# Kernel optimization log

Hardware: AMD Instinct MI355X
Metric: run time of the kernel (lower is better)

The kernel has to match this reference:

```python
import jax, jax.numpy as jnp
import numpy as np

EPS = 1e-8  # numerical guard in padded (masked) softmax denominator


def setup_inputs() -> dict:
    key = jax.random.key(0)
    k1, k2 = jax.random.split(key)
    B, N, D = 8, 2048, 3
    coordinates = jax.random.normal(k1, (B, N, D), dtype=jnp.float32)
    masks = (jax.random.uniform(k2, (B, N, N)) < 0.9).astype(jnp.float32)
    sigma = jnp.ones((1,), dtype=jnp.float32)  # NonNeg learned scalar
    return {"coordinates": coordinates, "masks": masks, "sigma": sigma}


def reference(coordinates, masks, sigma):
    # pairwise squared euclidean distances: ||xi||^2 - 2 xi.xj + ||xj||^2
    norms = jnp.sum(coordinates ** 2, axis=-1, keepdims=True)            # [B,N,1]
    inner = jnp.einsum('bnd,bmd->bnm', coordinates, coordinates)         # [B,N,N]
    distances = norms - 2.0 * inner + jnp.swapaxes(norms, -1, -2)        # [B,N,N]
    # Gaussian kernel
    A = jnp.exp(-distances / (sigma ** 2))                               # [B,N,N]
    # padded_softmax: mask then row-normalize (A is positive, so this is a
    # masked softmax over -d/sigma^2 along the last axis)
    A = A * masks
    return A / (jnp.sum(A, axis=-1, keepdims=True) + EPS)
```

## Files before the change

kernel.cpp:

```cpp
#include <hip/hip_runtime.h>
#include <math.h>


#define NN 2048
#define THREADS 256
#define RPB 8
#define EPS 1e-8f

typedef float nfloat4 __attribute__((ext_vector_type(4)));

__global__ __launch_bounds__(THREADS) void gauss_adj_kernel(
    const float* __restrict__ coords,
    const float* __restrict__ masks,
    const float* __restrict__ sigma,
    float* __restrict__ out)
{
    const int rows_base = blockIdx.x * RPB;
    const int b   = rows_base >> 11;
    const int ib  = rows_base & (NN - 1);
    const int tid = threadIdx.x;
    const int wave = tid >> 6;
    const int lane = tid & 63;

    __shared__ float srow[RPB * 3];
    __shared__ float red[2][4];

    const float* cb = coords + (size_t)b * NN * 3;
    if (tid < RPB * 3) srow[tid] = cb[ib * 3 + tid];

    const float4* cb4 = (const float4*)cb;
    float xs[2][4], ys[2][4], zs[2][4];
    #pragma unroll
    for (int c = 0; c < 2; ++c) {
        const int j4 = c * THREADS + tid;
        const float4 f0 = cb4[3 * j4 + 0];
        const float4 f1 = cb4[3 * j4 + 1];
        const float4 f2 = cb4[3 * j4 + 2];
        xs[c][0] = f0.x; ys[c][0] = f0.y; zs[c][0] = f0.z;
        xs[c][1] = f0.w; ys[c][1] = f1.x; zs[c][1] = f1.y;
        xs[c][2] = f1.z; ys[c][2] = f1.w; zs[c][2] = f2.x;
        xs[c][3] = f2.y; ys[c][3] = f2.z; zs[c][3] = f2.w;
    }

    const float s = sigma[0];
    const float inv_s2 = 1.0f / (s * s);

    __syncthreads();

    for (int r = 0; r < RPB; ++r) {
        const int row = rows_base + r;
        const float xi = srow[r * 3 + 0];
        const float yi = srow[r * 3 + 1];
        const float zi = srow[r * 3 + 2];

        const float4* mrow = (const float4*)(masks + (size_t)row * NN);

        float vals[2][4];
        float lsum = 0.0f;
        #pragma unroll
        for (int c = 0; c < 2; ++c) {
            const float4 m = mrow[c * THREADS + tid];
            const float mm[4] = {m.x, m.y, m.z, m.w};
            #pragma unroll
            for (int q = 0; q < 4; ++q) {
                const float dx = xi - xs[c][q];
                const float dy = yi - ys[c][q];
                const float dz = zi - zs[c][q];
                const float a = __expf(-(dx * dx + dy * dy + dz * dz) * inv_s2) * mm[q];
                vals[c][q] = a;
                lsum += a;
            }
        }

        #pragma unroll
        for (int off = 1; off < 64; off <<= 1)
            lsum += __shfl_xor(lsum, off, 64);
        if (lane == 0) red[r & 1][wave] = lsum;
        __syncthreads();
        const float tot = red[r & 1][0] + red[r & 1][1] + red[r & 1][2] + red[r & 1][3];
        const float inv = 1.0f / (tot + EPS);

        nfloat4* orow = (nfloat4*)(out + (size_t)row * NN);
        #pragma unroll
        for (int c = 0; c < 2; ++c) {
            nfloat4 o;
            o.x = vals[c][0] * inv;
            o.y = vals[c][1] * inv;
            o.z = vals[c][2] * inv;
            o.w = vals[c][3] * inv;
            __builtin_nontemporal_store(o, &orow[c * THREADS + tid]);
        }
    }
}

extern "C" void kernel_launch(void* const* d_in, const int* in_sizes, int n_in,
                              void* d_out, int out_size, void* d_ws, size_t ws_size,
                              hipStream_t stream) {
    const float* coords = (const float*)d_in[0];
    const float* masks  = (const float*)d_in[1];
    const float* sigma  = (const float*)d_in[2];
    float* out = (float*)d_out;

    const int B = in_sizes[0] / (NN * 3);
    const int rows = B * NN;
    gauss_adj_kernel<<<rows / RPB, THREADS, 0, stream>>>(coords, masks, sigma, out);
}
```

Before: 243.5 us.

## Batch row reductions into one barrier and recompute exps in a second pass

```diff
diff --git a/kernel.cpp b/kernel.cpp
--- a/kernel.cpp
+++ b/kernel.cpp
@@ -23,7 +23,7 @@
     const int lane = tid & 63;
 
     __shared__ float srow[RPB * 3];
-    __shared__ float red[2][4];
+    __shared__ float red[4][RPB];
 
     const float* cb = coords + (size_t)b * NN * 3;
     if (tid < RPB * 3) srow[tid] = cb[ib * 3 + tid];
@@ -47,47 +47,69 @@
 
     __syncthreads();
 
+    const float4* mbase = (const float4*)(masks + (size_t)rows_base * NN);
+
+    float lsum[RPB];
+    #pragma unroll
+    for (int r = 0; r < RPB; ++r) lsum[r] = 0.0f;
+
+    #pragma unroll
     for (int r = 0; r < RPB; ++r) {
-        const int row = rows_base + r;
         const float xi = srow[r * 3 + 0];
         const float yi = srow[r * 3 + 1];
         const float zi = srow[r * 3 + 2];
-
-        const float4* mrow = (const float4*)(masks + (size_t)row * NN);
-
-        float vals[2][4];
-        float lsum = 0.0f;
         #pragma unroll
         for (int c = 0; c < 2; ++c) {
-            const float4 m = mrow[c * THREADS + tid];
+            const float4 m = mbase[r * (NN / 4) + c * THREADS + tid];
             const float mm[4] = {m.x, m.y, m.z, m.w};
             #pragma unroll
             for (int q = 0; q < 4; ++q) {
                 const float dx = xi - xs[c][q];
                 const float dy = yi - ys[c][q];
                 const float dz = zi - zs[c][q];
-                const float a = __expf(-(dx * dx + dy * dy + dz * dz) * inv_s2) * mm[q];
-                vals[c][q] = a;
-                lsum += a;
+                lsum[r] += __expf(-(dx * dx + dy * dy + dz * dz) * inv_s2) * mm[q];
             }
         }
+    }
 
+    #pragma unroll
+    for (int r = 0; r < RPB; ++r) {
         #pragma unroll
         for (int off = 1; off < 64; off <<= 1)
-            lsum += __shfl_xor(lsum, off, 64);
-        if (lane == 0) red[r & 1][wave] = lsum;
-        __syncthreads();
-        const float tot = red[r & 1][0] + red[r & 1][1] + red[r & 1][2] + red[r & 1][3];
-        const float inv = 1.0f / (tot + EPS);
+            lsum[r] += __shfl_xor(lsum[r], off, 64);
+    }
+    if (lane == 0) {
+        #pragma unroll
+        for (int r = 0; r < RPB; ++r) red[wave][r] = lsum[r];
+    }
+    __syncthreads();
 
-        nfloat4* orow = (nfloat4*)(out + (size_t)row * NN);
+    float invv[RPB];
+    #pragma unroll
+    for (int r = 0; r < RPB; ++r)
+        invv[r] = 1.0f / (red[0][r] + red[1][r] + red[2][r] + red[3][r] + EPS);
+
+    #pragma unroll
+    for (int r = 0; r < RPB; ++r) {
+        const float xi = srow[r * 3 + 0];
+        const float yi = srow[r * 3 + 1];
+        const float zi = srow[r * 3 + 2];
+        const float inv = invv[r];
+        nfloat4* orow = (nfloat4*)(out + (size_t)(rows_base + r) * NN);
         #pragma unroll
         for (int c = 0; c < 2; ++c) {
+            const float4 m = mbase[r * (NN / 4) + c * THREADS + tid];
+            const float mm[4] = {m.x, m.y, m.z, m.w};
             nfloat4 o;
-            o.x = vals[c][0] * inv;
-            o.y = vals[c][1] * inv;
-            o.z = vals[c][2] * inv;
-            o.w = vals[c][3] * inv;
+            float ov[4];
+            #pragma unroll
+            for (int q = 0; q < 4; ++q) {
+                const float dx = xi - xs[c][q];
+                const float dy = yi - ys[c][q];
+                const float dz = zi - zs[c][q];
+                ov[q] = __expf(-(dx * dx + dy * dy + dz * dz) * inv_s2) * mm[q] * inv;
+            }
+            o.x = ov[0]; o.y = ov[1]; o.z = ov[2]; o.w = ov[3];
             __builtin_nontemporal_store(o, &orow[c * THREADS + tid]);
         }
     }
```

Measured after the change: 245.9 us. About the same (+1.0%).
